# Performance work log

Measured on AMD Instinct MI355X. Metric: run time of the kernel, lower is better.

## Reference

```python
import jax, jax.numpy as jnp
import numpy as np

DIM = 1024
NUM_HEADS = 16
HEAD_DIM = DIM // NUM_HEADS
INNER_ITR = 4
INNER_LR = 1.0
SCALE_QKV = 1.0


def setup_inputs() -> dict:
    key = jax.random.key(0)
    k1, k2, k3 = jax.random.split(key, 3)
    B, N, C = 8, 1024, DIM
    x = jax.random.normal(k1, (B, N, C), dtype=jnp.float32)
    # Xavier-uniform-ish scaled dense kernels
    w_qkv = jax.random.normal(k2, (C, 3 * C), dtype=jnp.float32) * (1.0 / np.sqrt(C))
    w_proj = jax.random.normal(k3, (C, C), dtype=jnp.float32) * (1.0 / np.sqrt(C))
    b_proj = jnp.zeros((C,), dtype=jnp.float32)
    return {"x": x, "w_qkv": w_qkv, "w_proj": w_proj, "b_proj": b_proj, "training": 0}


def _mttt_base(q, k, v):
    """MTTT 'base' inner loop: per (B,H) linear model W,b trained by
    INNER_ITR full-batch GD steps on MSE reconstruction of v from k,
    then applied to q. Shapes: q,k,v are (B, H, N, d)."""
    B, H, N, d = q.shape
    W = jnp.zeros((B, H, d, d), dtype=q.dtype)
    b = jnp.zeros((B, H, 1, d), dtype=q.dtype)
    invN = 1.0 / N
    for _ in range(INNER_ITR):  # small fixed iteration count
        pred = jnp.einsum('bhnd,bhde->bhne', k, W) + b   # (B,H,N,d)
        err = pred - v
        gW = jnp.einsum('bhnd,bhne->bhde', k, err) * invN
        gb = jnp.mean(err, axis=2, keepdims=True)
        W = W - INNER_LR * gW
        b = b - INNER_LR * gb
    return jnp.einsum('bhnd,bhde->bhne', q, W) + b       # (B,H,N,d)


def reference(x, w_qkv, w_proj, b_proj, training):
    B, N, C = x.shape
    H, d = NUM_HEADS, HEAD_DIM
    qkv = jnp.einsum('bnc,ce->bne', x, w_qkv)            # (B,N,3C), qkv_bias=False
    qkv = qkv.reshape(B, N, 3, H, d).transpose(2, 0, 3, 1, 4)  # (3,B,H,N,d)
    qkv = qkv * SCALE_QKV
    q, k, v = qkv[0], qkv[1], qkv[2]
    # qk_norm=False -> identity; scale_q=False -> no q scaling
    out = _mttt_base(q, k, v)                            # (B,H,N,d)
    out = out.transpose(0, 2, 1, 3).reshape(B, N, C)
    out = jnp.einsum('bnc,cd->bnd', out, w_proj) + b_proj
    # proj dropout deterministic (training=False)
    return out
```

## Files before the change

### kernel.cpp

```cpp
#include <hip/hip_runtime.h>


#define SEQ    1024
#define NBATCH 8
#define DIMC   1024
#define NHEAD  16
#define HDIM   64
#define MROWS  8192
#define NQKV   3072

typedef __attribute__((ext_vector_type(8))) __bf16 bf16x8;
typedef __attribute__((ext_vector_type(4))) float  f32x4;

__device__ __forceinline__ unsigned short f2b(float f) {
  union { float f; unsigned int u; } v; v.f = f;
  unsigned int r = (v.u + 0x7FFFu + ((v.u >> 16) & 1u)) >> 16;
  return (unsigned short)r;
}
__device__ __forceinline__ float b2f(unsigned short u) {
  union { unsigned int u; float f; } v; v.u = ((unsigned int)u) << 16;
  return v.f;
}

__device__ __forceinline__ void load_lds16(const void* g, void* l) {
  __builtin_amdgcn_global_load_lds(
      (__attribute__((address_space(1))) void*)(void*)(g),
      (__attribute__((address_space(3))) void*)(l), 16, 0, 0);
}

#define WAITVM(n_) do {                                                    \
    if ((n_) == 0) asm volatile("s_waitcnt vmcnt(0)" ::: "memory");        \
    else if ((n_) == 3) asm volatile("s_waitcnt vmcnt(3)" ::: "memory");   \
    else if ((n_) == 4) asm volatile("s_waitcnt vmcnt(4)" ::: "memory");   \
    else if ((n_) == 6) asm volatile("s_waitcnt vmcnt(6)" ::: "memory");   \
    else asm volatile("s_waitcnt vmcnt(8)" ::: "memory");                  \
  } while (0)

__global__ __launch_bounds__(256) void cvt_bf16(const float* __restrict__ in,
                                                unsigned short* __restrict__ out,
                                                int n4) {
  int i = blockIdx.x * 256 + threadIdx.x;
  if (i >= n4) return;
  float4 v = ((const float4*)in)[i];
  ushort4 o;
  o.x = f2b(v.x); o.y = f2b(v.y); o.z = f2b(v.z); o.w = f2b(v.w);
  ((ushort4*)out)[i] = o;
}

__global__ __launch_bounds__(256) void transpose_cvt(const float* __restrict__ in,
                                                     unsigned short* __restrict__ out,
                                                     int R, int Cc) {
  __shared__ unsigned short tile[32][33];
  int c0 = blockIdx.x * 32, r0 = blockIdx.y * 32;
  int tx = threadIdx.x, ty = threadIdx.y;
  for (int i = ty; i < 32; i += 8)
    tile[i][tx] = f2b(in[(size_t)(r0 + i) * Cc + c0 + tx]);
  __syncthreads();
  for (int i = ty; i < 32; i += 8)
    out[(size_t)(c0 + i) * R + r0 + tx] = tile[tx][i];
}

template <int BM, int STORE_F32>
__global__ __launch_bounds__(512, 2) void gemm8(const unsigned short* __restrict__ A,
                                                const unsigned short* __restrict__ BT,
                                                void* __restrict__ Cout,
                                                const float* __restrict__ bias,
                                                int N, int NBN) {
  constexpr int MI = BM / 32;
  constexpr int CA = BM / 128;
  constexpr int ABYTES = BM * 64;
  constexpr int SLAB = ABYTES + 16384;
  constexpr int CALLS = CA + 2;
  constexpr int WSTEADY = 2 * CALLS;
  constexpr int WTAIL = CALLS;

  extern __shared__ __align__(16) char lds[];

  const int tid = threadIdx.x;
  const int lane = tid & 63, wave = tid >> 6;
  const int wr = wave >> 2, wc = wave & 3;
  const int frow = lane & 15;
  const int g4 = lane >> 4;
  const int cswz = (g4 ^ (frow & 3)) * 16;

  const int cpx = gridDim.x >> 3;
  const int wg = (blockIdx.x & 7) * cpx + (blockIdx.x >> 3);
  const int bm = wg / NBN, bn = wg % NBN;
  const size_t m0 = (size_t)bm * BM, n0 = (size_t)bn * 256;

  const int srow = tid >> 2;
  const int schunk = ((tid & 3) ^ (srow & 3)) * 8;
  const unsigned short* srcA = A + (m0 + srow) * 1024 + schunk;
  const unsigned short* srcB = BT + (n0 + srow) * 1024 + schunk;
  const int wslot = wave * 1024;

  int aoff[MI], boff[4];
#pragma unroll
  for (int i = 0; i < MI; ++i) aoff[i] = (wr * (BM / 2) + i * 16 + frow) * 64 + cswz;
#pragma unroll
  for (int j = 0; j < 4; ++j)  boff[j] = ABYTES + (wc * 64 + j * 16 + frow) * 64 + cswz;

  f32x4 acc[MI][4];
  if (STORE_F32) {
#pragma unroll
    for (int j = 0; j < 4; ++j) {
      float4 bv = *(const float4*)&bias[n0 + wc * 64 + j * 16 + g4 * 4];
      f32x4 t; t[0] = bv.x; t[1] = bv.y; t[2] = bv.z; t[3] = bv.w;
#pragma unroll
      for (int i = 0; i < MI; ++i) acc[i][j] = t;
    }
  } else {
#pragma unroll
    for (int i = 0; i < MI; ++i)
#pragma unroll
      for (int j = 0; j < 4; ++j) acc[i][j] = f32x4{0.f, 0.f, 0.f, 0.f};
  }

  auto stage = [&](int s) {
    const int slot = s & 3;
    char* aL = lds + slot * SLAB + wslot;
    char* bL = lds + slot * SLAB + ABYTES + wslot;
    const unsigned short* aS = srcA + s * 32;
    const unsigned short* bS = srcB + s * 32;
    load_lds16(aS, aL);
    if (CA == 2) load_lds16(aS + 131072, aL + 8192);
    load_lds16(bS, bL);
    load_lds16(bS + 131072, bL + 8192);
  };

#define GEMM8_WINDOW(s_, wn_, dostage_) do {                                   \
    WAITVM(wn_);                                                               \
    __builtin_amdgcn_s_barrier();                                              \
    asm volatile("" ::: "memory");                                             \
    if (dostage_) stage((s_) + 3);                                             \
    const char* sa = lds + ((s_) & 3) * SLAB;                                  \
    bf16x8 af[MI], bq[4];                                                      \
    _Pragma("unroll") for (int i = 0; i < MI; ++i)                             \
      af[i] = *(const bf16x8*)(sa + aoff[i]);                                  \
    _Pragma("unroll") for (int j = 0; j < 4; ++j)                              \
      bq[j] = *(const bf16x8*)(sa + boff[j]);                                  \
    __builtin_amdgcn_s_setprio(1);                                             \
    _Pragma("unroll") for (int i = 0; i < MI; ++i)                             \
    _Pragma("unroll") for (int j = 0; j < 4; ++j)                              \
      acc[i][j] = __builtin_amdgcn_mfma_f32_16x16x32_bf16(bq[j], af[i],        \
                                                          acc[i][j], 0, 0, 0); \
    __builtin_amdgcn_s_setprio(0);                                             \
  } while (0)

  stage(0); stage(1); stage(2);
  for (int s = 0; s < 30; ++s) GEMM8_WINDOW(s, WSTEADY, s < 29);
  GEMM8_WINDOW(30, WTAIL, false);
  GEMM8_WINDOW(31, 0, false);
#undef GEMM8_WINDOW

  const size_t mbase = m0 + wr * (BM / 2) + frow;
  const size_t nbase = n0 + wc * 64 + g4 * 4;
  if (STORE_F32) {
    float* C = (float*)Cout;
#pragma unroll
    for (int i = 0; i < MI; ++i)
#pragma unroll
      for (int j = 0; j < 4; ++j) {
        float4 o; o.x = acc[i][j][0]; o.y = acc[i][j][1];
        o.z = acc[i][j][2]; o.w = acc[i][j][3];
        *(float4*)&C[(mbase + i * 16) * N + nbase + j * 16] = o;
      }
  } else {
    unsigned short* C = (unsigned short*)Cout;
#pragma unroll
    for (int i = 0; i < MI; ++i)
#pragma unroll
      for (int j = 0; j < 4; ++j) {
        ushort4 o; o.x = f2b(acc[i][j][0]); o.y = f2b(acc[i][j][1]);
        o.z = f2b(acc[i][j][2]); o.w = f2b(acc[i][j][3]);
        *(ushort4*)&C[(mbase + i * 16) * N + nbase + j * 16] = o;
      }
  }
}

__global__ __launch_bounds__(256) void transpose_kv(const unsigned short* __restrict__ qkvb,
                                                    unsigned short* __restrict__ kt,
                                                    unsigned short* __restrict__ vt) {
  __shared__ unsigned short tile[64][80];
  const int nc = blockIdx.x * 64;
  const int bh = blockIdx.y;
  const int which = blockIdx.z;
  const int b = bh >> 4, h = bh & 15;
  const int tid = threadIdx.x;
  const unsigned short* src = qkvb + (size_t)(b * SEQ + nc) * NQKV + (which + 1) * DIMC + h * HDIM;
  for (int idx = tid; idx < 512; idx += 256) {
    int rr = idx >> 3, ss = (idx & 7) * 8;
    *(uint4*)&tile[rr][ss] = *(const uint4*)&src[(size_t)rr * NQKV + ss];
  }
  __syncthreads();
  unsigned short* dst = (which ? vt : kt) + (size_t)bh * HDIM * SEQ;
  for (int idx = tid; idx < 512; idx += 256) {
    int dd = idx >> 3, ns = (idx & 7) * 8;
    alignas(16) unsigned short tmp[8];
#pragma unroll
    for (int jj = 0; jj < 8; ++jj) tmp[jj] = tile[ns + jj][dd];
    *(uint4*)&dst[(size_t)dd * SEQ + nc + ns] = *(const uint4*)tmp;
  }
}

__global__ __launch_bounds__(256) void stats_gd(const unsigned short* __restrict__ kt,
                                                const unsigned short* __restrict__ vt,
                                                unsigned short* __restrict__ Wtb,
                                                float* __restrict__ bvec) {
  __shared__ float Gs[64][68];
  __shared__ float Ps[64][68];
  __shared__ float Ws[64][68];
  __shared__ float mkp[4][64], mvp[4][64];
  __shared__ float mks[64], mvs[64], bs[64];

  const int bh = blockIdx.x;
  const int tid = threadIdx.x;
  const int lane = tid & 63, wave = tid >> 6;
  const unsigned short* kb = kt + (size_t)bh * HDIM * SEQ;
  const unsigned short* vb = vt + (size_t)bh * HDIM * SEQ;
  const int frow = lane & 15;
  const int fk = (lane >> 4) * 8;

  f32x4 accG[4], accP[4];
#pragma unroll
  for (int j = 0; j < 4; ++j) {
    accG[j] = f32x4{0.f, 0.f, 0.f, 0.f};
    accP[j] = f32x4{0.f, 0.f, 0.f, 0.f};
  }
  for (int nb = 0; nb < SEQ; nb += 32) {
    bf16x8 af = *(const bf16x8*)&kb[(size_t)(wave * 16 + frow) * SEQ + nb + fk];
    bf16x8 kf[4], vf[4];
#pragma unroll
    for (int j = 0; j < 4; ++j)
      kf[j] = *(const bf16x8*)&kb[(size_t)(j * 16 + frow) * SEQ + nb + fk];
#pragma unroll
    for (int j = 0; j < 4; ++j)
      vf[j] = *(const bf16x8*)&vb[(size_t)(j * 16 + frow) * SEQ + nb + fk];
#pragma unroll
    for (int j = 0; j < 4; ++j) {
      accG[j] = __builtin_amdgcn_mfma_f32_16x16x32_bf16(af, kf[j], accG[j], 0, 0, 0);
      accP[j] = __builtin_amdgcn_mfma_f32_16x16x32_bf16(af, vf[j], accP[j], 0, 0, 0);
    }
  }
  const float invN = 1.0f / (float)SEQ;
  const int orow = wave * 16 + (lane >> 4) * 4;
#pragma unroll
  for (int j = 0; j < 4; ++j)
#pragma unroll
    for (int r = 0; r < 4; ++r) {
      Gs[orow + r][j * 16 + frow] = accG[j][r] * invN;
      Ps[orow + r][j * 16 + frow] = accP[j][r] * invN;
    }

  {
    float sk_ = 0.f, sv_ = 0.f;
    const unsigned short* kr = &kb[(size_t)lane * SEQ + wave * 256];
    const unsigned short* vr = &vb[(size_t)lane * SEQ + wave * 256];
    for (int nn = 0; nn < 256; nn += 8) {
      uint4 a = *(const uint4*)&kr[nn];
      uint4 c = *(const uint4*)&vr[nn];
      const unsigned short* pa = (const unsigned short*)&a;
      const unsigned short* pc = (const unsigned short*)&c;
#pragma unroll
      for (int jj = 0; jj < 8; ++jj) { sk_ += b2f(pa[jj]); sv_ += b2f(pc[jj]); }
    }
    mkp[wave][lane] = sk_;
    mvp[wave][lane] = sv_;
  }
  __syncthreads();

  const int r = tid >> 2;
  const int c0 = (tid & 3) * 16;
  if (tid < 64) {
    mks[tid] = (mkp[0][tid] + mkp[1][tid] + mkp[2][tid] + mkp[3][tid]) * invN;
    mvs[tid] = (mvp[0][tid] + mvp[1][tid] + mvp[2][tid] + mvp[3][tid]) * invN;
    bs[tid] = 0.f;
  }
#pragma unroll
  for (int c = 0; c < 16; ++c) Ws[r][c0 + c] = 0.f;
  __syncthreads();

  for (int it = 0; it < 4; ++it) {
    float wn[16];
#pragma unroll
    for (int c = 0; c < 16; ++c)
      wn[c] = Ws[r][c0 + c] + Ps[r][c0 + c] - mks[r] * bs[c0 + c];
    for (int j = 0; j < 64; ++j) {
      float g = Gs[r][j];
#pragma unroll
      for (int c = 0; c < 16; ++c) wn[c] -= g * Ws[j][c0 + c];
    }
    float bn = 0.f;
    if (tid < 64) {
      bn = mvs[tid];
      for (int j = 0; j < 64; ++j) bn -= mks[j] * Ws[j][tid];
    }
    __syncthreads();
#pragma unroll
    for (int c = 0; c < 16; ++c) Ws[r][c0 + c] = wn[c];
    if (tid < 64) bs[tid] = bn;
    __syncthreads();
  }

  unsigned short* wout = Wtb + (size_t)bh * HDIM * HDIM;
#pragma unroll
  for (int c = 0; c < 16; ++c)
    wout[(size_t)(c0 + c) * HDIM + r] = f2b(Ws[r][c0 + c]);
  if (tid < 64) bvec[(size_t)bh * HDIM + tid] = bs[tid];
}

__global__ __launch_bounds__(256) void attn_qw(const unsigned short* __restrict__ qkvb,
                                               const unsigned short* __restrict__ Wtb,
                                               const float* __restrict__ bvec,
                                               unsigned short* __restrict__ attnb) {
  const int h = blockIdx.y;
  const int m0 = blockIdx.x * 128;
  const int bh = ((m0 >> 10) << 4) + h;
  const int tid = threadIdx.x;
  const int lane = tid & 63, wave = tid >> 6;
  const int frow = lane & 15;
  const int fk = (lane >> 4) * 8;

  f32x4 acc[2][4];
#pragma unroll
  for (int j = 0; j < 4; ++j) {
    float bv = bvec[(size_t)bh * HDIM + j * 16 + frow];
    f32x4 t; t[0] = bv; t[1] = bv; t[2] = bv; t[3] = bv;
    acc[0][j] = t; acc[1][j] = t;
  }

  const unsigned short* qbase = qkvb + (size_t)(m0 + wave * 32) * NQKV + h * HDIM;
  const unsigned short* wbase = Wtb + (size_t)bh * HDIM * HDIM;
#pragma unroll
  for (int s = 0; s < 2; ++s) {
    bf16x8 af[2], wf[4];
#pragma unroll
    for (int i = 0; i < 2; ++i)
      af[i] = *(const bf16x8*)&qbase[(size_t)(i * 16 + frow) * NQKV + s * 32 + fk];
#pragma unroll
    for (int j = 0; j < 4; ++j)
      wf[j] = *(const bf16x8*)&wbase[(size_t)(j * 16 + frow) * HDIM + s * 32 + fk];
#pragma unroll
    for (int i = 0; i < 2; ++i)
#pragma unroll
      for (int j = 0; j < 4; ++j)
        acc[i][j] = __builtin_amdgcn_mfma_f32_16x16x32_bf16(af[i], wf[j], acc[i][j], 0, 0, 0);
  }

  const int orow = m0 + wave * 32 + (lane >> 4) * 4;
#pragma unroll
  for (int i = 0; i < 2; ++i)
#pragma unroll
    for (int j = 0; j < 4; ++j)
#pragma unroll
      for (int rr = 0; rr < 4; ++rr)
        attnb[(size_t)(orow + i * 16 + rr) * DIMC + h * HDIM + j * 16 + frow] = f2b(acc[i][j][rr]);
}

extern "C" void kernel_launch(void* const* d_in, const int* in_sizes, int n_in,
                              void* d_out, int out_size, void* d_ws, size_t ws_size,
                              hipStream_t stream) {
  const float* x      = (const float*)d_in[0];
  const float* w_qkv  = (const float*)d_in[1];
  const float* w_proj = (const float*)d_in[2];
  const float* b_proj = (const float*)d_in[3];

  char* ws = (char*)d_ws;
  unsigned short* xb    = (unsigned short*)(ws + 0);
  unsigned short* wqT   = (unsigned short*)(ws + 16777216);
  unsigned short* wpT   = (unsigned short*)(ws + 23068672);
  unsigned short* qkvb  = (unsigned short*)(ws + 25165824);
  unsigned short* kt    = (unsigned short*)(ws + 75497472);
  unsigned short* vt    = (unsigned short*)(ws + 92274688);
  unsigned short* attnb = (unsigned short*)(ws + 109051904);
  unsigned short* Wtb   = (unsigned short*)(ws + 125829120);
  float*          bvec  = (float*)(ws + 126877696);
  if (ws_size < (size_t)126910464) return;

  hipFuncSetAttribute((const void*)gemm8<256, 0>,
                      hipFuncAttributeMaxDynamicSharedMemorySize, 131072);
  hipFuncSetAttribute((const void*)gemm8<128, 1>,
                      hipFuncAttributeMaxDynamicSharedMemorySize, 131072);

  cvt_bf16<<<8192, 256, 0, stream>>>(x, xb, MROWS * DIMC / 4);
  transpose_cvt<<<dim3(96, 32), dim3(32, 8), 0, stream>>>(w_qkv, wqT, 1024, 3072);
  transpose_cvt<<<dim3(32, 32), dim3(32, 8), 0, stream>>>(w_proj, wpT, 1024, 1024);
  gemm8<256, 0><<<dim3(384), dim3(512), 131072, stream>>>(xb, wqT, qkvb, nullptr, NQKV, 12);
  transpose_kv<<<dim3(16, 128, 2), 256, 0, stream>>>(qkvb, kt, vt);
  stats_gd<<<128, 256, 0, stream>>>(kt, vt, Wtb, bvec);
  attn_qw<<<dim3(64, 16), 256, 0, stream>>>(qkvb, Wtb, bvec, attnb);
  gemm8<128, 1><<<dim3(256), dim3(512), 98304, stream>>>(attnb, wpT, d_out, b_proj, DIMC, 4);
}
```

Baseline: 200.3 us.

## Restructure bf16 GEMM into 8-wave ping-pong schedule with K=64 double-buffered tiles

Rewrites both projection GEMMs to use 64-wide K tiles in two LDS buffers instead of 32-wide tiles in four slots. The main loop is split into quadrant phases: each wave reads part of its A/B fragments, hits a barrier, then issues a block of MFMAs. Global-to-LDS stages are interleaved between phases, and the LDS swizzle moves to an 8-way XOR pattern. The goal is to overlap LDS reads and global loads with matrix math and cut bank conflicts, at the cost of many more barriers per iteration. The 128-row variant needs 96KB of LDS, which it already requested.

```diff
diff --git a/kernel.cpp b/kernel.cpp
--- a/kernel.cpp
+++ b/kernel.cpp
@@ -28,9 +28,15 @@
       (__attribute__((address_space(3))) void*)(l), 16, 0, 0);
 }
 
+#define FENCE asm volatile("" ::: "memory")
+#define BAR   __builtin_amdgcn_s_barrier()
+#define LGKM0 do { asm volatile("s_waitcnt lgkmcnt(0)" ::: "memory"); \
+                   __builtin_amdgcn_sched_barrier(0); } while (0)
+#define PRIO1 __builtin_amdgcn_s_setprio(1)
+#define PRIO0 __builtin_amdgcn_s_setprio(0)
+
 #define WAITVM(n_) do {                                                    \
     if ((n_) == 0) asm volatile("s_waitcnt vmcnt(0)" ::: "memory");        \
-    else if ((n_) == 3) asm volatile("s_waitcnt vmcnt(3)" ::: "memory");   \
     else if ((n_) == 4) asm volatile("s_waitcnt vmcnt(4)" ::: "memory");   \
     else if ((n_) == 6) asm volatile("s_waitcnt vmcnt(6)" ::: "memory");   \
     else asm volatile("s_waitcnt vmcnt(8)" ::: "memory");                  \
@@ -61,44 +67,41 @@
 }
 
 template <int BM, int STORE_F32>
-__global__ __launch_bounds__(512, 2) void gemm8(const unsigned short* __restrict__ A,
-                                                const unsigned short* __restrict__ BT,
-                                                void* __restrict__ Cout,
-                                                const float* __restrict__ bias,
-                                                int N, int NBN) {
+__global__ __launch_bounds__(512, 2) void gemm_p8(const unsigned short* __restrict__ A,
+                                                  const unsigned short* __restrict__ BT,
+                                                  void* __restrict__ Cout,
+                                                  const float* __restrict__ bias,
+                                                  int N, int NBN) {
   constexpr int MI = BM / 32;
-  constexpr int CA = BM / 128;
-  constexpr int ABYTES = BM * 64;
-  constexpr int SLAB = ABYTES + 16384;
-  constexpr int CALLS = CA + 2;
-  constexpr int WSTEADY = 2 * CALLS;
-  constexpr int WTAIL = CALLS;
-
-  extern __shared__ __align__(16) char lds[];
+  constexpr int MH = MI / 2;
+  constexpr int ABYTES = BM * 128;
+  constexpr int BBYTES = 32768;
+  constexpr int BUFB = ABYTES + BBYTES;
+  constexpr int ACALLS = BM / 128;
+  constexpr int NTC = 4 + 2 * ACALLS;
+
+  extern __shared__ __align__(16) char ldsb[];
 
   const int tid = threadIdx.x;
   const int lane = tid & 63, wave = tid >> 6;
   const int wr = wave >> 2, wc = wave & 3;
   const int frow = lane & 15;
   const int g4 = lane >> 4;
-  const int cswz = (g4 ^ (frow & 3)) * 16;
+  const int cz0 = (g4 ^ (lane & 7)) * 16;
+  const int cz1 = ((4 | g4) ^ (lane & 7)) * 16;
 
   const int cpx = gridDim.x >> 3;
   const int wg = (blockIdx.x & 7) * cpx + (blockIdx.x >> 3);
   const int bm = wg / NBN, bn = wg % NBN;
   const size_t m0 = (size_t)bm * BM, n0 = (size_t)bn * 256;
 
-  const int srow = tid >> 2;
-  const int schunk = ((tid & 3) ^ (srow & 3)) * 8;
-  const unsigned short* srcA = A + (m0 + srow) * 1024 + schunk;
-  const unsigned short* srcB = BT + (n0 + srow) * 1024 + schunk;
-  const int wslot = wave * 1024;
-
-  int aoff[MI], boff[4];
-#pragma unroll
-  for (int i = 0; i < MI; ++i) aoff[i] = (wr * (BM / 2) + i * 16 + frow) * 64 + cswz;
-#pragma unroll
-  for (int j = 0; j < 4; ++j)  boff[j] = ABYTES + (wc * 64 + j * 16 + frow) * 64 + cswz;
+  const int srow = tid >> 3;
+  const int scol = ((tid & 7) ^ ((tid >> 3) & 7)) * 8;
+  const unsigned short* srcA = A + (m0 + srow) * 1024 + scol;
+  const unsigned short* srcB = BT + (n0 + srow) * 1024 + scol;
+
+  const int aBase = (wr * (BM / 2) + frow) * 128;
+  const int bBase = (wc * 64 + frow) * 128;
 
   f32x4 acc[MI][4];
   if (STORE_F32) {
@@ -116,42 +119,87 @@
       for (int j = 0; j < 4; ++j) acc[i][j] = f32x4{0.f, 0.f, 0.f, 0.f};
   }
 
-  auto stage = [&](int s) {
-    const int slot = s & 3;
-    char* aL = lds + slot * SLAB + wslot;
-    char* bL = lds + slot * SLAB + ABYTES + wslot;
-    const unsigned short* aS = srcA + s * 32;
-    const unsigned short* bS = srcB + s * 32;
-    load_lds16(aS, aL);
-    if (CA == 2) load_lds16(aS + 131072, aL + 8192);
-    load_lds16(bS, bL);
-    load_lds16(bS + 131072, bL + 8192);
+  auto stageA = [&](int buf_, int h_, int tt_) {
+    char* dst = ldsb + buf_ * BUFB + h_ * (ABYTES / 2) + wave * 1024;
+    const unsigned short* s = srcA + (size_t)(h_ * (BM / 2)) * 1024 + tt_ * 64;
+    load_lds16(s, dst);
+    if constexpr (ACALLS == 2) load_lds16(s + 65536, dst + 8192);
   };
-
-#define GEMM8_WINDOW(s_, wn_, dostage_) do {                                   \
-    WAITVM(wn_);                                                               \
-    __builtin_amdgcn_s_barrier();                                              \
-    asm volatile("" ::: "memory");                                             \
-    if (dostage_) stage((s_) + 3);                                             \
-    const char* sa = lds + ((s_) & 3) * SLAB;                                  \
-    bf16x8 af[MI], bq[4];                                                      \
-    _Pragma("unroll") for (int i = 0; i < MI; ++i)                             \
-      af[i] = *(const bf16x8*)(sa + aoff[i]);                                  \
-    _Pragma("unroll") for (int j = 0; j < 4; ++j)                              \
-      bq[j] = *(const bf16x8*)(sa + boff[j]);                                  \
-    __builtin_amdgcn_s_setprio(1);                                             \
-    _Pragma("unroll") for (int i = 0; i < MI; ++i)                             \
-    _Pragma("unroll") for (int j = 0; j < 4; ++j)                              \
-      acc[i][j] = __builtin_amdgcn_mfma_f32_16x16x32_bf16(bq[j], af[i],        \
-                                                          acc[i][j], 0, 0, 0); \
-    __builtin_amdgcn_s_setprio(0);                                             \
+  auto stageB = [&](int buf_, int h_, int tt_) {
+    char* dst = ldsb + buf_ * BUFB + ABYTES + h_ * 16384 + wave * 1024;
+    const unsigned short* s = srcB + (size_t)(h_ * 128) * 1024 + tt_ * 64;
+    load_lds16(s, dst);
+    load_lds16(s + 65536, dst + 8192);
+  };
+
+#define READ_A(buf_, mh_, dst_) do {                                     \
+    const char* ab_ = ldsb + (buf_) * BUFB + aBase + (mh_) * (MH * 2048);\
+    _Pragma("unroll") for (int fi = 0; fi < MH; ++fi) {                  \
+      dst_[fi][0] = *(const bf16x8*)(ab_ + fi * 2048 + cz0);             \
+      dst_[fi][1] = *(const bf16x8*)(ab_ + fi * 2048 + cz1); }           \
   } while (0)
 
-  stage(0); stage(1); stage(2);
-  for (int s = 0; s < 30; ++s) GEMM8_WINDOW(s, WSTEADY, s < 29);
-  GEMM8_WINDOW(30, WTAIL, false);
-  GEMM8_WINDOW(31, 0, false);
-#undef GEMM8_WINDOW
+#define READ_B(buf_, nh_, dst_) do {                                     \
+    const char* bb_ = ldsb + (buf_) * BUFB + ABYTES + bBase + (nh_) * 4096;\
+    _Pragma("unroll") for (int fj = 0; fj < 2; ++fj) {                   \
+      dst_[fj][0] = *(const bf16x8*)(bb_ + fj * 2048 + cz0);             \
+      dst_[fj][1] = *(const bf16x8*)(bb_ + fj * 2048 + cz1); }           \
+  } while (0)
+
+#define MFMAQ(mh_, nh_, bb_)                                             \
+    _Pragma("unroll") for (int fi = 0; fi < MH; ++fi)                    \
+    _Pragma("unroll") for (int fj = 0; fj < 2; ++fj)                     \
+    _Pragma("unroll") for (int kk = 0; kk < 2; ++kk)                     \
+      acc[(mh_) * MH + fi][(nh_) * 2 + fj] =                             \
+        __builtin_amdgcn_mfma_f32_16x16x32_bf16(bb_[fj][kk], aq[fi][kk], \
+            acc[(mh_) * MH + fi][(nh_) * 2 + fj], 0, 0, 0)
+
+  stageB(0, 0, 0); stageB(0, 1, 0); stageA(0, 0, 0); stageA(0, 1, 0);
+  stageB(1, 0, 1); stageB(1, 1, 1); stageA(1, 0, 1); stageA(1, 1, 1);
+  WAITVM(NTC);
+  FENCE; BAR;
+
+#pragma unroll 1
+  for (int it = 0; it < 8; ++it) {
+    const int st = (it < 7);
+    const int t2 = 2 * it + 2, t3 = 2 * it + 3;
+    bf16x8 aq[MH][2], b0[2][2], b1[2][2];
+    READ_A(0, 0, aq); READ_B(0, 0, b0);
+    FENCE; BAR; LGKM0;
+    PRIO1; MFMAQ(0, 0, b0); PRIO0; FENCE; BAR;
+    READ_B(0, 1, b1);
+    FENCE; BAR; LGKM0;
+    PRIO1; MFMAQ(0, 1, b1); PRIO0; FENCE; BAR;
+    READ_A(0, 1, aq);
+    if (st) stageB(0, 0, t2);
+    FENCE; BAR; LGKM0;
+    PRIO1; MFMAQ(1, 0, b0); PRIO0; FENCE; BAR;
+    if (st) stageB(0, 1, t2);
+    FENCE; BAR; LGKM0;
+    PRIO1; MFMAQ(1, 1, b1); PRIO0;
+    if (st) WAITVM(4); else WAITVM(0);
+    FENCE; BAR;
+    READ_A(1, 0, aq); READ_B(1, 0, b0);
+    if (st) stageA(0, 0, t2);
+    FENCE; BAR; LGKM0;
+    PRIO1; MFMAQ(0, 0, b0); PRIO0; FENCE; BAR;
+    READ_B(1, 1, b1);
+    if (st) stageA(0, 1, t2);
+    FENCE; BAR; LGKM0;
+    PRIO1; MFMAQ(0, 1, b1); PRIO0; FENCE; BAR;
+    READ_A(1, 1, aq);
+    if (st) stageB(1, 0, t3);
+    FENCE; BAR; LGKM0;
+    PRIO1; MFMAQ(1, 0, b0); PRIO0; FENCE; BAR;
+    if (st) { stageB(1, 1, t3); stageA(1, 0, t3); stageA(1, 1, t3); }
+    FENCE; BAR; LGKM0;
+    PRIO1; MFMAQ(1, 1, b1); PRIO0;
+    WAITVM(NTC);
+    FENCE; BAR;
+  }
+#undef READ_A
+#undef READ_B
+#undef MFMAQ
 
   const size_t mbase = m0 + wr * (BM / 2) + frow;
   const size_t nbase = n0 + wc * 64 + g4 * 4;
@@ -377,17 +425,17 @@
   float*          bvec  = (float*)(ws + 126877696);
   if (ws_size < (size_t)126910464) return;
 
-  hipFuncSetAttribute((const void*)gemm8<256, 0>,
+  hipFuncSetAttribute((const void*)gemm_p8<256, 0>,
                       hipFuncAttributeMaxDynamicSharedMemorySize, 131072);
-  hipFuncSetAttribute((const void*)gemm8<128, 1>,
+  hipFuncSetAttribute((const void*)gemm_p8<128, 1>,
                       hipFuncAttributeMaxDynamicSharedMemorySize, 131072);
 
   cvt_bf16<<<8192, 256, 0, stream>>>(x, xb, MROWS * DIMC / 4);
   transpose_cvt<<<dim3(96, 32), dim3(32, 8), 0, stream>>>(w_qkv, wqT, 1024, 3072);
   transpose_cvt<<<dim3(32, 32), dim3(32, 8), 0, stream>>>(w_proj, wpT, 1024, 1024);
-  gemm8<256, 0><<<dim3(384), dim3(512), 131072, stream>>>(xb, wqT, qkvb, nullptr, NQKV, 12);
+  gemm_p8<256, 0><<<dim3(384), dim3(512), 131072, stream>>>(xb, wqT, qkvb, nullptr, NQKV, 12);
   transpose_kv<<<dim3(16, 128, 2), 256, 0, stream>>>(qkvb, kt, vt);
   stats_gd<<<128, 256, 0, stream>>>(kt, vt, Wtb, bvec);
   attn_qw<<<dim3(64, 16), 256, 0, stream>>>(qkvb, Wtb, bvec, attnb);
-  gemm8<128, 1><<<dim3(256), dim3(512), 98304, stream>>>(attnb, wpT, d_out, b_proj, DIMC, 4);
-}
+  gemm_p8<128, 1><<<dim3(256), dim3(512), 98304, stream>>>(attnb, wpT, d_out, b_proj, DIMC, 4);
+}
```

Result: no change. 198.0 us (-1.1%).
